# Performance work log

Measured on AMD Instinct MI355X. Metric: run time of the kernel, lower is better.

Reference implementation:

```python
import jax, jax.numpy as jnp
import numpy as np

N = 262144   # number of units (batched instances of the module)
G = 128      # universe_field side length
D = 128      # dimension
RADIUS = 3   # min(3, G//2) == 3

# First D=128 neighborhood offsets in the original triple-loop order (i-major, j, k)
_grid = np.stack(np.meshgrid(np.arange(-RADIUS, RADIUS + 1),
                             np.arange(-RADIUS, RADIUS + 1),
                             np.arange(-RADIUS, RADIUS + 1), indexing='ij'), -1).reshape(-1, 3)[:D]
OI = jnp.asarray(_grid[:, 0], dtype=jnp.int32)
OJ = jnp.asarray(_grid[:, 1], dtype=jnp.int32)
OK = jnp.asarray(_grid[:, 2], dtype=jnp.int32)


def setup_inputs() -> dict:
    key = jax.random.key(0)
    ks = jax.random.split(key, 8)
    return {
        'universe_field': jax.random.normal(ks[0], (G, G, G), jnp.float32),
        'positions': jax.random.uniform(ks[1], (N, 3), jnp.float32) * G,
        'signatures': jax.random.normal(ks[2], (N, D), jnp.float32),
        'offsets': jax.random.normal(ks[3], (N, 3), jnp.float32) * 0.1,
        'W1': jax.random.normal(ks[4], (2 * D, D), jnp.float32) * (1.0 / np.sqrt(2 * D)),
        'b1': jax.random.normal(ks[5], (D,), jnp.float32) * 0.01,
        'W2': jax.random.normal(ks[6], (D, D), jnp.float32) * (1.0 / np.sqrt(D)),
        'b2': jax.random.normal(ks[7], (D,), jnp.float32) * 0.01,
    }


def _sample_local(field, pos):
    # pos: [N,3] float; truncate to int (torch .long()) then clamp, like the original
    pc = jnp.clip(jax.lax.stop_gradient(pos).astype(jnp.int32), 0, G - 1)  # [N,3]
    xx = jnp.clip(pc[:, 0:1] + OI[None, :], 0, G - 1)  # [N,D]
    yy = jnp.clip(pc[:, 1:2] + OJ[None, :], 0, G - 1)
    zz = jnp.clip(pc[:, 2:3] + OK[None, :], 0, G - 1)
    return field[xx, yy, zz]  # [N,D] gathered local field (343 points truncated to D)


def _stability(field, pos, signatures, W1, b1, W2, b2):
    local = _sample_local(field, pos)                       # [N,D]
    combined = jnp.concatenate([signatures, local], axis=-1)  # [N,2D]
    h = jnp.tanh(combined @ W1 + b1)                        # [N,D]
    resp = h @ W2 + b2                                      # [N,D]
    return jnp.linalg.norm(resp - signatures, axis=-1)      # [N]


def reference(universe_field, positions, signatures, offsets, W1, b1, W2, b2):
    stab_old = _stability(universe_field, positions, signatures, W1, b1, W2, b2)
    test_pos = positions + offsets
    stab_new = _stability(universe_field, test_pos, signatures, W1, b1, W2, b2)
    accept = stab_new <= stab_old                           # revert move if new_stab > old_stab
    final_pos = jnp.where(accept[:, None], test_pos, positions)
    stability = jnp.where(accept, stab_new, stab_old)
    return stability, final_pos
```

## Files before the change

kernel.cpp:

```cpp
#include <hip/hip_runtime.h>
#include <hip/hip_bf16.h>

#define NU 262144
#define GG 128
#define PG 134
#define DD 128

typedef __attribute__((ext_vector_type(8))) short short8;
typedef __attribute__((ext_vector_type(4))) float f32x4;

union Frag { short8 s; unsigned u[4]; };

__device__ __forceinline__ unsigned short f2b(float f) {
  union { float f; unsigned u; } v; v.f = f;
  unsigned r = v.u + 0x7fffu + ((v.u >> 16) & 1u);
  return (unsigned short)(r >> 16);
}
__device__ __forceinline__ unsigned cvtpk(float lo, float hi) {
  unsigned r;
  asm("v_cvt_pk_bf16_f32 %0, %1, %2" : "=v"(r) : "v"(lo), "v"(hi));
  return r;
}
__device__ __forceinline__ float unplo(unsigned w) {
  union { unsigned u; float f; } v; v.u = w << 16; return v.f;
}
__device__ __forceinline__ float unphi(unsigned w) {
  union { unsigned u; float f; } v; v.u = w & 0xffff0000u; return v.f;
}

__device__ __forceinline__ float fast_tanh(float x) {
  float e = __expf(fabsf(x) * 2.0f);
  float r = __frcp_rn(e + 1.0f);
  return copysignf(fmaf(-2.0f, r, 1.0f), x);
}

struct alignas(16) RowdT { int v[20]; };
static constexpr RowdT mkrowd() {
  RowdT t{};
  for (int r = 0; r < 20; ++r) {
    int rr = (r < 18) ? r : 18;
    int di = (rr < 18) ? (-3 + rr / 7) : -1;
    int dj = (rr < 18) ? (-3 + rr % 7) : 1;
    t.v[r] = (di * PG + dj) * PG - 3;
  }
  return t;
}
__device__ constexpr RowdT ROWD = mkrowd();

__global__ void prep_field(const float* __restrict__ f, unsigned short* __restrict__ fp) {
  int idx = blockIdx.x * 256 + threadIdx.x;
  if (idx >= PG * PG * PG) return;
  int z = idx % PG, t = idx / PG;
  int y = t % PG, x = t / PG;
  int xx = min(max(x - 3, 0), GG - 1);
  int yy = min(max(y - 3, 0), GG - 1);
  int zz = min(max(z - 3, 0), GG - 1);
  fp[idx] = f2b(f[(xx * GG + yy) * GG + zz]);
}

__global__ void prep_w(const float* __restrict__ W1, const float* __restrict__ W2,
                       unsigned short* __restrict__ wall) {
  int idx = blockIdx.x * 256 + threadIdx.x;
  if (idx >= 6656) return;
  int kt = idx >> 9, nt = (idx >> 6) & 7, ln = idx & 63;
  int n = nt * 16 + (ln & 15), lg = ln >> 4;
  short8 s;
  if (kt < 4) {
    int k0 = kt * 32 + lg * 8;
#pragma unroll
    for (int j = 0; j < 8; ++j) s[j] = (short)f2b(W1[(k0 + j) * DD + n]);
  } else if (kt < 9) {
    int r = (kt - 4) * 4 + lg;
#pragma unroll
    for (int j = 0; j < 8; ++j) {
      bool valid = (r < 18 && j < 7) || (r == 18 && j < 2);
      int row = 128 + ((r < 18) ? (r * 7 + j) : (126 + j));
      s[j] = valid ? (short)f2b(W1[row * DD + n]) : (short)0;
    }
  } else {
    int k0 = (kt - 9) * 32 + lg * 8;
#pragma unroll
    for (int j = 0; j < 8; ++j) s[j] = (short)f2b(W2[(k0 + j) * DD + n]);
  }
  ((short8*)wall)[idx] = s;
}

__global__ __launch_bounds__(512, 4) void atu_main(
    const float* __restrict__ pos, const float* __restrict__ sig,
    const float* __restrict__ offs,
    const float* __restrict__ b1, const float* __restrict__ b2,
    const unsigned short* __restrict__ fpad, const unsigned short* __restrict__ wall,
    float* __restrict__ out_stab, float* __restrict__ out_pos)
{
  __shared__ unsigned short ldsw[2][8192];
  __shared__ alignas(16) unsigned short ns[8][2048];
  const int tid  = threadIdx.x;
  const int lane = tid & 63;
  const int lg   = lane >> 4, lm = lane & 15;
  const int wid  = tid >> 6;
  int bid = blockIdx.x;
  int swz = (bid & 7) * 256 + (bid >> 3);
  const int ub = swz * 128 + wid * 16;
  const int un = ub + lm;
  char* nsb = (char*)&ns[wid][0];
  const char* wallb = (const char*)wall;
  const char* fpadb = (const char*)fpad;

  int abase[2];
  {
    float px = pos[un * 3 + 0], py = pos[un * 3 + 1], pz = pos[un * 3 + 2];
    float qx = px + offs[un * 3 + 0], qy = py + offs[un * 3 + 1], qz = pz + offs[un * 3 + 2];
    int ax = min(max((int)px, 0), GG - 1), ay = min(max((int)py, 0), GG - 1), az = min(max((int)pz, 0), GG - 1);
    int bx = min(max((int)qx, 0), GG - 1), by = min(max((int)qy, 0), GG - 1), bz = min(max((int)qz, 0), GG - 1);
    abase[0] = ((ax + 3) * PG + (ay + 3)) * PG + (az + 3);
    abase[1] = ((bx + 3) * PG + (by + 3)) * PG + (bz + 3);
  }

#define GLL2(KTA, H)                                                              \
  __builtin_amdgcn_global_load_lds(                                               \
      (const unsigned*)(wallb + (((KTA) * 512 + tid) * 16)),                      \
      (unsigned*)((char*)&ldsw[H][0] + wid * 1024), 16, 0, 0);                    \
  __builtin_amdgcn_global_load_lds(                                               \
      (const unsigned*)(wallb + ((((KTA) + 1) * 512 + tid) * 16)),                \
      (unsigned*)((char*)&ldsw[H][0] + 8192 + wid * 1024), 16, 0, 0);

#define GLL1(KTA, H)                                                              \
  __builtin_amdgcn_global_load_lds(                                               \
      (const unsigned*)(wallb + (((KTA) * 512 + tid) * 16)),                      \
      (unsigned*)((char*)&ldsw[H][0] + wid * 1024), 16, 0, 0);

  GLL2(0, 0)
  f32x4 spa = *(const f32x4*)(sig + (size_t)un * DD + lg * 8);
  f32x4 spb = *(const f32x4*)(sig + (size_t)un * DD + lg * 8 + 4);
  short8 rw[5][2];
#pragma unroll
  for (int k = 0; k < 5; ++k) {
    int rd = ROWD.v[k * 4 + lg];
    rw[k][0] = *(const short8*)(fpadb + 2 * (size_t)(abase[0] + rd));
    rw[k][1] = *(const short8*)(fpadb + 2 * (size_t)(abase[1] + rd));
  }

  f32x4 acc[8][2];
#pragma unroll
  for (int nt = 0; nt < 8; ++nt) acc[nt][0] = *(const f32x4*)(b1 + nt * 16 + lg * 4);
  f32x4 acc2[8][2];
  unsigned Q[2][8][2];

  __syncthreads();

#define SIG_KT(KT, HALF)                                                          \
  {                                                                               \
    f32x4 na, nb;                                                                 \
    if ((KT) < 3) {                                                               \
      na = *(const f32x4*)(sig + (size_t)un * DD + ((KT) + 1) * 32 + lg * 8);     \
      nb = *(const f32x4*)(sig + (size_t)un * DD + ((KT) + 1) * 32 + lg * 8 + 4); \
    }                                                                             \
    Frag B;                                                                       \
    B.u[0] = cvtpk(spa[0], spa[1]); B.u[1] = cvtpk(spa[2], spa[3]);               \
    B.u[2] = cvtpk(spb[0], spb[1]); B.u[3] = cvtpk(spb[2], spb[3]);               \
    *(short8*)(nsb + ((KT) * 4 + lg) * 256 + lm * 16) = B.s;                      \
    const char* buf = (const char*)&ldsw[HALF][0] + (((KT) & 1) ? 8192 : 0);      \
    _Pragma("unroll")                                                             \
    for (int nt = 0; nt < 8; ++nt) {                                              \
      short8 af = *(const short8*)(buf + (nt * 64 + lane) * 16);                  \
      acc[nt][0] = __builtin_amdgcn_mfma_f32_16x16x32_bf16(af, B.s, acc[nt][0], 0, 0, 0); \
    }                                                                             \
    if ((KT) < 3) { spa = na; spb = nb; }                                         \
  }

#define ROW_KT(KT, HALF)                                                          \
  {                                                                               \
    const char* buf = (const char*)&ldsw[HALF][0] + (((KT) & 1) ? 8192 : 0);      \
    _Pragma("unroll")                                                             \
    for (int nt = 0; nt < 8; ++nt) {                                              \
      short8 af = *(const short8*)(buf + (nt * 64 + lane) * 16);                  \
      acc[nt][0] = __builtin_amdgcn_mfma_f32_16x16x32_bf16(af, rw[(KT) - 4][0], acc[nt][0], 0, 0, 0); \
      acc[nt][1] = __builtin_amdgcn_mfma_f32_16x16x32_bf16(af, rw[(KT) - 4][1], acc[nt][1], 0, 0, 0); \
    }                                                                             \
  }

#define G2_KT(KT, HALF)                                                           \
  {                                                                               \
    constexpr int kb = (KT) - 9;                                                  \
    Frag W[2];                                                                    \
    _Pragma("unroll")                                                             \
    for (int ut = 0; ut < 2; ++ut) {                                              \
      int qa0 = (int)Q[ut][2 * kb][0],     qa1 = (int)Q[ut][2 * kb][1];           \
      int qb0 = (int)Q[ut][2 * kb + 1][0], qb1 = (int)Q[ut][2 * kb + 1][1];       \
      int r00 = __builtin_amdgcn_ds_bpermute(ad0, qa0);                           \
      int r01 = __builtin_amdgcn_ds_bpermute(ad0, qa1);                           \
      int r10 = __builtin_amdgcn_ds_bpermute(ad1, qa0);                           \
      int r11 = __builtin_amdgcn_ds_bpermute(ad1, qa1);                           \
      int s00 = __builtin_amdgcn_ds_bpermute(ad0, qb0);                           \
      int s01 = __builtin_amdgcn_ds_bpermute(ad0, qb1);                           \
      int s10 = __builtin_amdgcn_ds_bpermute(ad1, qb0);                           \
      int s11 = __builtin_amdgcn_ds_bpermute(ad1, qb1);                           \
      W[ut].u[0] = (unsigned)(hi ? s00 : r00);                                    \
      W[ut].u[1] = (unsigned)(hi ? s01 : r01);                                    \
      W[ut].u[2] = (unsigned)(hi ? s10 : r10);                                    \
      W[ut].u[3] = (unsigned)(hi ? s11 : r11);                                    \
    }                                                                             \
    const char* buf = (const char*)&ldsw[HALF][0] + (((KT) & 1) ? 8192 : 0);      \
    _Pragma("unroll")                                                             \
    for (int nt = 0; nt < 8; ++nt) {                                              \
      short8 af = *(const short8*)(buf + (nt * 64 + lane) * 16);                  \
      acc2[nt][0] = __builtin_amdgcn_mfma_f32_16x16x32_bf16(af, W[0].s, acc2[nt][0], 0, 0, 0); \
      acc2[nt][1] = __builtin_amdgcn_mfma_f32_16x16x32_bf16(af, W[1].s, acc2[nt][1], 0, 0, 0); \
    }                                                                             \
  }

  const int ad0 = ((((2 * lg) & 3) * 16) + lm) * 4;
  const int ad1 = ((((2 * lg + 1) & 3) * 16) + lm) * 4;
  const bool hi = (lg >= 2);

  GLL2(2, 1)
  SIG_KT(0, 0) SIG_KT(1, 0)
  __syncthreads();

  GLL2(4, 0)
  SIG_KT(2, 1) SIG_KT(3, 1)
  __syncthreads();

#pragma unroll
  for (int nt = 0; nt < 8; ++nt) acc[nt][1] = acc[nt][0];

  GLL2(6, 1)
  ROW_KT(4, 0) ROW_KT(5, 0)
  __syncthreads();

  GLL2(8, 0)
  ROW_KT(6, 1) ROW_KT(7, 1)
  __syncthreads();

  GLL2(10, 1)
  ROW_KT(8, 0)

#pragma unroll
  for (int nt = 0; nt < 8; ++nt) {
#pragma unroll
    for (int ut = 0; ut < 2; ++ut) {
      float h0 = fast_tanh(acc[nt][ut][0]);
      float h1 = fast_tanh(acc[nt][ut][1]);
      float h2 = fast_tanh(acc[nt][ut][2]);
      float h3 = fast_tanh(acc[nt][ut][3]);
      Q[ut][nt][0] = cvtpk(h0, h1);
      Q[ut][nt][1] = cvtpk(h2, h3);
    }
  }
#pragma unroll
  for (int nt = 0; nt < 8; ++nt) {
    f32x4 b2v = *(const f32x4*)(b2 + nt * 16 + lg * 4);
    acc2[nt][0] = b2v; acc2[nt][1] = b2v;
  }

  G2_KT(9, 0)
  __syncthreads();

  GLL1(12, 0)
  G2_KT(10, 1) G2_KT(11, 1)
  __syncthreads();

  G2_KT(12, 0)

  float ssq[2] = {0.f, 0.f};
#pragma unroll
  for (int nt = 0; nt < 8; ++nt) {
    unsigned long long w64 = *(const unsigned long long*)
        (nsb + (nt * 2 + (lg >> 1)) * 256 + lm * 16 + (lg & 1) * 8);
    unsigned w0 = (unsigned)w64, w1 = (unsigned)(w64 >> 32);
    float sv0 = unplo(w0), sv1 = unphi(w0);
    float sv2 = unplo(w1), sv3 = unphi(w1);
#pragma unroll
    for (int ut = 0; ut < 2; ++ut) {
      float d0 = acc2[nt][ut][0] - sv0;
      float d1 = acc2[nt][ut][1] - sv1;
      float d2 = acc2[nt][ut][2] - sv2;
      float d3 = acc2[nt][ut][3] - sv3;
      ssq[ut] = fmaf(d0, d0, ssq[ut]);
      ssq[ut] = fmaf(d1, d1, ssq[ut]);
      ssq[ut] = fmaf(d2, d2, ssq[ut]);
      ssq[ut] = fmaf(d3, d3, ssq[ut]);
    }
  }
  ssq[0] += __shfl_xor(ssq[0], 16, 64); ssq[0] += __shfl_xor(ssq[0], 32, 64);
  ssq[1] += __shfl_xor(ssq[1], 16, 64); ssq[1] += __shfl_xor(ssq[1], 32, 64);

  if (lane < 16) {
    float px = pos[un * 3 + 0], py = pos[un * 3 + 1], pz = pos[un * 3 + 2];
    float ox = offs[un * 3 + 0], oy = offs[un * 3 + 1], oz = offs[un * 3 + 2];
    bool ok = ssq[1] <= ssq[0];
    out_stab[un] = sqrtf(ok ? ssq[1] : ssq[0]);
    out_pos[un * 3 + 0] = ok ? px + ox : px;
    out_pos[un * 3 + 1] = ok ? py + oy : py;
    out_pos[un * 3 + 2] = ok ? pz + oz : pz;
  }
#undef GLL2
#undef GLL1
#undef SIG_KT
#undef ROW_KT
#undef G2_KT
}

extern "C" void kernel_launch(void* const* d_in, const int* in_sizes, int n_in,
                              void* d_out, int out_size, void* d_ws, size_t ws_size,
                              hipStream_t stream) {
  const float* field = (const float*)d_in[0];
  const float* pos   = (const float*)d_in[1];
  const float* sig   = (const float*)d_in[2];
  const float* offs  = (const float*)d_in[3];
  const float* W1    = (const float*)d_in[4];
  const float* b1    = (const float*)d_in[5];
  const float* W2    = (const float*)d_in[6];
  const float* b2    = (const float*)d_in[7];
  float* out_stab = (float*)d_out;
  float* out_pos  = out_stab + NU;

  char* ws = (char*)d_ws;
  unsigned short* fpad = (unsigned short*)ws;
  unsigned short* wall = (unsigned short*)(ws + 4812800);

  prep_field<<<(PG * PG * PG + 255) / 256, 256, 0, stream>>>(field, fpad);
  prep_w<<<26, 256, 0, stream>>>(W1, W2, wall);
  atu_main<<<NU / 128, 512, 0, stream>>>(pos, sig, offs, b1, b2,
                                         fpad, wall, out_stab, out_pos);
}
```

Before: 134.8 us.

## Prefetch all weight k-tiles into eight LDS slots and cut barriers

Replaces the double-buffered weight staging with eight LDS slots, so the first eight weight k-tiles are prefetched at kernel start and the remaining five are loaded after the first barrier. This reduces the number of block-wide barriers from six to two and removes per-step load/compute interleaving. The cost is doubling the weight LDS footprint, which raises per-block LDS use and can reduce the number of resident blocks per CU.

Measured after the change: 156.1 us. +15.8%, slower.

```diff
diff --git a/kernel.cpp b/kernel.cpp
--- a/kernel.cpp
+++ b/kernel.cpp
@@ -92,7 +92,7 @@
     const unsigned short* __restrict__ fpad, const unsigned short* __restrict__ wall,
     float* __restrict__ out_stab, float* __restrict__ out_pos)
 {
-  __shared__ unsigned short ldsw[2][8192];
+  __shared__ unsigned short ldsw[8][4096];
   __shared__ alignas(16) unsigned short ns[8][2048];
   const int tid  = threadIdx.x;
   const int lane = tid & 63;
@@ -106,6 +106,14 @@
   const char* wallb = (const char*)wall;
   const char* fpadb = (const char*)fpad;
 
+#define GLL(KT, SLOT)                                                             \
+  __builtin_amdgcn_global_load_lds(                                               \
+      (const unsigned*)(wallb + (((KT) * 512 + tid) * 16)),                       \
+      (unsigned*)((char*)&ldsw[SLOT][0] + wid * 1024), 16, 0, 0);
+
+  GLL(0, 0) GLL(1, 1) GLL(2, 2) GLL(3, 3)
+  GLL(4, 4) GLL(5, 5) GLL(6, 6) GLL(7, 7)
+
   int abase[2];
   {
     float px = pos[un * 3 + 0], py = pos[un * 3 + 1], pz = pos[un * 3 + 2];
@@ -116,20 +124,6 @@
     abase[1] = ((bx + 3) * PG + (by + 3)) * PG + (bz + 3);
   }
 
-#define GLL2(KTA, H)                                                              \
-  __builtin_amdgcn_global_load_lds(                                               \
-      (const unsigned*)(wallb + (((KTA) * 512 + tid) * 16)),                      \
-      (unsigned*)((char*)&ldsw[H][0] + wid * 1024), 16, 0, 0);                    \
-  __builtin_amdgcn_global_load_lds(                                               \
-      (const unsigned*)(wallb + ((((KTA) + 1) * 512 + tid) * 16)),                \
-      (unsigned*)((char*)&ldsw[H][0] + 8192 + wid * 1024), 16, 0, 0);
-
-#define GLL1(KTA, H)                                                              \
-  __builtin_amdgcn_global_load_lds(                                               \
-      (const unsigned*)(wallb + (((KTA) * 512 + tid) * 16)),                      \
-      (unsigned*)((char*)&ldsw[H][0] + wid * 1024), 16, 0, 0);
-
-  GLL2(0, 0)
   f32x4 spa = *(const f32x4*)(sig + (size_t)un * DD + lg * 8);
   f32x4 spb = *(const f32x4*)(sig + (size_t)un * DD + lg * 8 + 4);
   short8 rw[5][2];
@@ -148,7 +142,7 @@
 
   __syncthreads();
 
-#define SIG_KT(KT, HALF)                                                          \
+#define SIG_KT(KT, SLOT)                                                          \
   {                                                                               \
     f32x4 na, nb;                                                                 \
     if ((KT) < 3) {                                                               \
@@ -159,7 +153,7 @@
     B.u[0] = cvtpk(spa[0], spa[1]); B.u[1] = cvtpk(spa[2], spa[3]);               \
     B.u[2] = cvtpk(spb[0], spb[1]); B.u[3] = cvtpk(spb[2], spb[3]);               \
     *(short8*)(nsb + ((KT) * 4 + lg) * 256 + lm * 16) = B.s;                      \
-    const char* buf = (const char*)&ldsw[HALF][0] + (((KT) & 1) ? 8192 : 0);      \
+    const char* buf = (const char*)&ldsw[SLOT][0];                                \
     _Pragma("unroll")                                                             \
     for (int nt = 0; nt < 8; ++nt) {                                              \
       short8 af = *(const short8*)(buf + (nt * 64 + lane) * 16);                  \
@@ -168,9 +162,9 @@
     if ((KT) < 3) { spa = na; spb = nb; }                                         \
   }
 
-#define ROW_KT(KT, HALF)                                                          \
+#define ROW_KT(KT, SLOT)                                                          \
   {                                                                               \
-    const char* buf = (const char*)&ldsw[HALF][0] + (((KT) & 1) ? 8192 : 0);      \
+    const char* buf = (const char*)&ldsw[SLOT][0];                                \
     _Pragma("unroll")                                                             \
     for (int nt = 0; nt < 8; ++nt) {                                              \
       short8 af = *(const short8*)(buf + (nt * 64 + lane) * 16);                  \
@@ -179,7 +173,7 @@
     }                                                                             \
   }
 
-#define G2_KT(KT, HALF)                                                           \
+#define G2_KT(KT, SLOT)                                                           \
   {                                                                               \
     constexpr int kb = (KT) - 9;                                                  \
     Frag W[2];                                                                    \
@@ -200,7 +194,7 @@
       W[ut].u[2] = (unsigned)(hi ? s10 : r10);                                    \
       W[ut].u[3] = (unsigned)(hi ? s11 : r11);                                    \
     }                                                                             \
-    const char* buf = (const char*)&ldsw[HALF][0] + (((KT) & 1) ? 8192 : 0);      \
+    const char* buf = (const char*)&ldsw[SLOT][0];                                \
     _Pragma("unroll")                                                             \
     for (int nt = 0; nt < 8; ++nt) {                                              \
       short8 af = *(const short8*)(buf + (nt * 64 + lane) * 16);                  \
@@ -213,26 +207,21 @@
   const int ad1 = ((((2 * lg + 1) & 3) * 16) + lm) * 4;
   const bool hi = (lg >= 2);
 
-  GLL2(2, 1)
-  SIG_KT(0, 0) SIG_KT(1, 0)
+  SIG_KT(0, 0) SIG_KT(1, 1) SIG_KT(2, 2) SIG_KT(3, 3)
+
+#pragma unroll
+  for (int nt = 0; nt < 8; ++nt) acc[nt][1] = acc[nt][0];
+
+  ROW_KT(4, 4) ROW_KT(5, 5)
+
   __syncthreads();
 
-  GLL2(4, 0)
-  SIG_KT(2, 1) SIG_KT(3, 1)
+  GLL(8, 0) GLL(9, 1) GLL(10, 2) GLL(11, 3) GLL(12, 4)
+
+  ROW_KT(6, 6) ROW_KT(7, 7)
+
   __syncthreads();
 
-#pragma unroll
-  for (int nt = 0; nt < 8; ++nt) acc[nt][1] = acc[nt][0];
-
-  GLL2(6, 1)
-  ROW_KT(4, 0) ROW_KT(5, 0)
-  __syncthreads();
-
-  GLL2(8, 0)
-  ROW_KT(6, 1) ROW_KT(7, 1)
-  __syncthreads();
-
-  GLL2(10, 1)
   ROW_KT(8, 0)
 
 #pragma unroll
@@ -253,14 +242,7 @@
     acc2[nt][0] = b2v; acc2[nt][1] = b2v;
   }
 
-  G2_KT(9, 0)
-  __syncthreads();
-
-  GLL1(12, 0)
-  G2_KT(10, 1) G2_KT(11, 1)
-  __syncthreads();
-
-  G2_KT(12, 0)
+  G2_KT(9, 1) G2_KT(10, 2) G2_KT(11, 3) G2_KT(12, 4)
 
   float ssq[2] = {0.f, 0.f};
 #pragma unroll
@@ -294,8 +276,7 @@
     out_pos[un * 3 + 1] = ok ? py + oy : py;
     out_pos[un * 3 + 2] = ok ? pz + oz : pz;
   }
-#undef GLL2
-#undef GLL1
+#undef GLL
 #undef SIG_KT
 #undef ROW_KT
 #undef G2_KT
```
